# Performance work log

Measured on AMD Instinct MI355X. Metric: run time of the kernel, lower is better.

The kernel has to match this reference:

```python
import jax, jax.numpy as jnp
import numpy as np

C = 256  # channels
B, H, W = 16, 64, 64


def _conv1x1(x, w, b):
    # x: [B,Cin,H,W], w: [Cout,Cin], b: [Cout] -> [B,Cout,H,W]
    return jnp.einsum('bchw,oc->bohw', x, w) + b[None, :, None, None]


def _axis_attn(x, wq, bq, wf, bf, axis):
    # axis: -1 for 'W', -2 for 'H'
    qkv = _conv1x1(x, wq, bq)                      # [B,1+2C,H,W]
    query = qkv[:, :1]                             # [B,1,H,W]
    key = qkv[:, 1:1 + C]                          # [B,C,H,W]
    value = qkv[:, 1 + C:]                         # [B,C,H,W]
    scores = jax.nn.softmax(query, axis=axis)      # softmax over spatial axis
    context = jnp.sum(key * scores, axis=axis, keepdims=True)  # [B,C,H,1] or [B,C,1,W]
    gate = jax.nn.sigmoid(value)
    out = x + gate * context                       # broadcast over reduced axis
    return _conv1x1(out, wf, bf)


def setup_inputs() -> dict:
    key = jax.random.key(0)
    ks = jax.random.split(key, 5)
    s_qkv = 1.0 / np.sqrt(C)
    s_fus = 1.0 / np.sqrt(C)
    return {
        'x': jax.random.normal(ks[0], (B, C, H, W), dtype=jnp.float32),
        'qkvW_w': jax.random.normal(ks[1], (1 + 2 * C, C), dtype=jnp.float32) * s_qkv,
        'qkvW_b': jnp.zeros((1 + 2 * C,), dtype=jnp.float32),
        'qkvH_w': jax.random.normal(ks[2], (1 + 2 * C, C), dtype=jnp.float32) * s_qkv,
        'qkvH_b': jnp.zeros((1 + 2 * C,), dtype=jnp.float32),
        'fusW_w': jax.random.normal(ks[3], (C, C), dtype=jnp.float32) * s_fus,
        'fusW_b': jnp.zeros((C,), dtype=jnp.float32),
        'fusH_w': jax.random.normal(ks[4], (C, C), dtype=jnp.float32) * s_fus,
        'fusH_b': jnp.zeros((C,), dtype=jnp.float32),
    }


def reference(x, qkvW_w, qkvW_b, qkvH_w, qkvH_b, fusW_w, fusW_b, fusH_w, fusH_b):
    x_w = _axis_attn(x, qkvW_w, qkvW_b, fusW_w, fusW_b, axis=-1)
    x_h = _axis_attn(x_w, qkvH_w, qkvH_b, fusH_w, fusH_b, axis=-2)
    return x_h
```

## Files before the change

kernel.cpp:

```cpp
#include <hip/hip_runtime.h>

typedef unsigned short u16;
typedef unsigned int u32;
typedef __attribute__((ext_vector_type(8))) short bf16x8;
typedef __attribute__((ext_vector_type(4))) float f32x4;

__device__ __forceinline__ u16 f2bf(float f) {
    u32 u = __builtin_bit_cast(u32, f);
    u += 0x7FFFu + ((u >> 16) & 1u);
    return (u16)(u >> 16);
}
__device__ __forceinline__ float bf2f(u16 s) {
    u32 u = ((u32)s) << 16;
    return __builtin_bit_cast(float, u);
}
__device__ __forceinline__ float sigm(float x) {
    return 1.0f / (1.0f + __expf(-x));
}
__device__ __forceinline__ void gload16(const u16* g, u16* l) {
    __builtin_amdgcn_global_load_lds(
        (const __attribute__((address_space(1))) void*)g,
        (__attribute__((address_space(3))) void*)l, 16, 0, 0);
}

__global__ __launch_bounds__(256) void transpose_in(const float* __restrict__ x,
                                                    u16* __restrict__ xp) {
    __shared__ float tile[64][65];
    int bid = blockIdx.x;
    int ct = bid & 3, h = (bid >> 2) & 63, b = bid >> 8;
    int t = threadIdx.x;
    int tr = t >> 4, tc = t & 15;
    const float* src = x + (((size_t)(b * 256 + ct * 64) * 64 + h) * 64);
#pragma unroll
    for (int i = 0; i < 4; ++i) {
        int c = tr + i * 16;
        float4 v = *(const float4*)(src + (size_t)c * 4096 + tc * 4);
        tile[c][tc * 4 + 0] = v.x;
        tile[c][tc * 4 + 1] = v.y;
        tile[c][tc * 4 + 2] = v.z;
        tile[c][tc * 4 + 3] = v.w;
    }
    __syncthreads();
    u16* dst = xp + ((size_t)((b * 64 + h) * 64)) * 256 + ct * 64;
#pragma unroll
    for (int i = 0; i < 4; ++i) {
        int w = tr + i * 16;
        ushort4 o;
        o.x = f2bf(tile[tc * 4 + 0][w]);
        o.y = f2bf(tile[tc * 4 + 1][w]);
        o.z = f2bf(tile[tc * 4 + 2][w]);
        o.w = f2bf(tile[tc * 4 + 3][w]);
        *(ushort4*)(dst + (size_t)w * 256 + tc * 4) = o;
    }
}

__global__ __launch_bounds__(256) void prep_w(const float* __restrict__ qw,
                                              const float* __restrict__ qb,
                                              const float* __restrict__ fw,
                                              const float* __restrict__ fb,
                                              float* __restrict__ wq0,
                                              u16* __restrict__ wkv,
                                              float* __restrict__ bkv,
                                              u16* __restrict__ wf,
                                              float* __restrict__ bff) {
    int i = blockIdx.x * 256 + threadIdx.x;
    if (i < 513 * 256) {
        int o = i >> 8, c = i & 255;
        float v = qw[i];
        if (o == 0) wq0[c] = v;
        else        wkv[(size_t)(o - 1) * 256 + c] = f2bf(v);
    }
    if (i < 65536) wf[i] = f2bf(fw[i]);
    if (i < 512)   bkv[i] = qb[i + 1];
    if (i < 256)   bff[i] = fb[i];
}

template <int AXIS>
__global__ __launch_bounds__(512, 4) void qkv_attn(
    const u16* __restrict__ A, const u16* __restrict__ Bw,
    const float* __restrict__ bkv, const float* __restrict__ wq0,
    u16* __restrict__ G) {
    __shared__ alignas(16) u16 Asm[128 * 256];
    __shared__ float ql[128];
    __shared__ float sc[128];
    __shared__ alignas(16) float ctxs[2][256];
    int t = threadIdx.x, lane = t & 63, wv = t >> 6;
    int beta = blockIdx.x;
    auto prow = [&](int r) -> size_t {
        if (AXIS == 0) return (size_t)beta * 128 + r;
        else           return (size_t)(beta >> 5) * 4096 + (size_t)(r & 63) * 64 +
                              ((beta & 31) * 2) + (r >> 6);
    };
    {
#pragma unroll
        for (int i = 0; i < 8; ++i) {
            int row = i * 16 + wv * 2 + (lane >> 5);
            int slot = (lane & 31) ^ (row & 7);
            gload16(A + prow(row) * 256 + slot * 8, &Asm[(i * 16 + wv * 2) * 256]);
        }
    }
    __syncthreads();
    {
        int row = t >> 2, g = t & 3;
        const float* wp = wq0 + g * 64;
        float a = 0.f;
#pragma unroll
        for (int cc = 0; cc < 8; ++cc) {
            int slot = (g * 8 + cc) ^ (row & 7);
            bf16x8 v = *(const bf16x8*)&Asm[row * 256 + slot * 8];
#pragma unroll
            for (int j = 0; j < 8; ++j) a += bf2f((u16)v[j]) * wp[cc * 8 + j];
        }
        a += __shfl_xor(a, 1);
        a += __shfl_xor(a, 2);
        if (g == 0) ql[row] = a;
    }
    __syncthreads();
    if (t < 128) {
        float qv = ql[t];
        float m = qv;
#pragma unroll
        for (int off = 32; off > 0; off >>= 1) m = fmaxf(m, __shfl_xor(m, off));
        float e = __expf(qv - m);
        float s = e;
#pragma unroll
        for (int off = 32; off > 0; off >>= 1) s += __shfl_xor(s, off);
        sc[t] = e / s;
    }
    __syncthreads();
    int rowhalf = wv >> 2, chq = wv & 3;
    int arow = lane & 15, kgrp = lane >> 4;
    float sv[4];
#pragma unroll
    for (int ni = 0; ni < 4; ++ni) sv[ni] = sc[rowhalf * 64 + ni * 16 + arow];
    for (int ot = 0; ot < 4; ++ot) {
        f32x4 zero = {0.f, 0.f, 0.f, 0.f};
        f32x4 acc[2][4];
#pragma unroll
        for (int mi = 0; mi < 2; ++mi)
#pragma unroll
            for (int ni = 0; ni < 4; ++ni) acc[mi][ni] = zero;
#pragma unroll
        for (int ks = 0; ks < 8; ++ks) {
            bf16x8 aw[2], bx[4];
#pragma unroll
            for (int mi = 0; mi < 2; ++mi)
                aw[mi] = *(const bf16x8*)(Bw +
                    (size_t)(ot * 128 + chq * 32 + mi * 16 + arow) * 256 +
                    ks * 32 + kgrp * 8);
#pragma unroll
            for (int ni = 0; ni < 4; ++ni) {
                int p = rowhalf * 64 + ni * 16 + arow;
                int slot = (ks * 4 + kgrp) ^ (p & 7);
                bx[ni] = *(const bf16x8*)&Asm[p * 256 + slot * 8];
            }
#pragma unroll
            for (int mi = 0; mi < 2; ++mi)
#pragma unroll
                for (int ni = 0; ni < 4; ++ni)
                    acc[mi][ni] = __builtin_amdgcn_mfma_f32_16x16x32_bf16(
                        aw[mi], bx[ni], acc[mi][ni], 0, 0, 0);
        }
        if (ot < 2) {
#pragma unroll
            for (int mi = 0; mi < 2; ++mi) {
                int c = ot * 128 + chq * 32 + mi * 16 + kgrp * 4;
                f32x4 red;
#pragma unroll
                for (int r = 0; r < 4; ++r) {
                    float s = 0.f;
#pragma unroll
                    for (int ni = 0; ni < 4; ++ni) s += acc[mi][ni][r] * sv[ni];
                    s += __shfl_xor(s, 1);
                    s += __shfl_xor(s, 2);
                    s += __shfl_xor(s, 4);
                    s += __shfl_xor(s, 8);
                    red[r] = s;
                }
                if (arow == 0) {
                    f32x4 bv = *(const f32x4*)&bkv[c];
                    red[0] += bv[0]; red[1] += bv[1];
                    red[2] += bv[2]; red[3] += bv[3];
                    *(f32x4*)&ctxs[rowhalf][c] = red;
                }
            }
        } else {
#pragma unroll
            for (int mi = 0; mi < 2; ++mi) {
                int cv = (ot - 2) * 128 + chq * 32 + mi * 16 + kgrp * 4;
                f32x4 bv = *(const f32x4*)&bkv[256 + cv];
                f32x4 cxv = *(const f32x4*)&ctxs[rowhalf][cv];
#pragma unroll
                for (int ni = 0; ni < 4; ++ni) {
                    int p = rowhalf * 64 + ni * 16 + arow;
                    int slot = (cv >> 3) ^ (p & 7);
                    ushort4 xv = *(const ushort4*)&Asm[p * 256 + slot * 8 + (cv & 7)];
                    ushort4 o;
                    o.x = f2bf(bf2f(xv.x) + sigm(acc[mi][ni][0] + bv[0]) * cxv[0]);
                    o.y = f2bf(bf2f(xv.y) + sigm(acc[mi][ni][1] + bv[1]) * cxv[1]);
                    o.z = f2bf(bf2f(xv.z) + sigm(acc[mi][ni][2] + bv[2]) * cxv[2]);
                    o.w = f2bf(bf2f(xv.w) + sigm(acc[mi][ni][3] + bv[3]) * cxv[3]);
                    *(ushort4*)(G + prow(p) * 256 + cv) = o;
                }
            }
        }
        if (ot == 1) __syncthreads();
    }
}

template <int MODE>
__global__ __launch_bounds__(256, 2) void gemm_k(
    const u16* __restrict__ A, const u16* __restrict__ Bw,
    const float* __restrict__ bias,
    u16* __restrict__ bOut, float* __restrict__ fOut) {
    int h = blockIdx.x;
    int xcd = h & 7, slot = h >> 3;
    int otile = slot & 1, ptile = xcd * 64 + (slot >> 1);
    __shared__ alignas(16) u16 Asm[128 * 64];
    __shared__ alignas(16) u16 Bsm[128 * 64];
    int p0 = ptile * 128, o0 = otile * 128;
    int t = threadIdx.x, lane = t & 63, wv = t >> 6;
    int wm = (wv >> 1) * 64, wn = (wv & 1) * 64;
    int l7 = lane & 7;
    int srcoff = (lane >> 3) * 256 + (((lane & 7) ^ (lane >> 3)) * 8);
    int arow = lane & 15, kgrp = lane >> 4;
    f32x4 zero = {0.f, 0.f, 0.f, 0.f};
    f32x4 acc[4][4];
#pragma unroll
    for (int i = 0; i < 4; ++i)
#pragma unroll
        for (int jj = 0; jj < 4; ++jj) acc[i][jj] = zero;

    for (int k0 = 0; k0 < 256; k0 += 64) {
        __syncthreads();
#pragma unroll
        for (int it = 0; it < 4; ++it) {
            int r0 = it * 32 + wv * 8;
            gload16(A + (size_t)(p0 + r0) * 256 + k0 + srcoff, &Asm[r0 * 64]);
            gload16(Bw + (size_t)(o0 + r0) * 256 + k0 + srcoff, &Bsm[r0 * 64]);
        }
        __syncthreads();
#pragma unroll
        for (int kk = 0; kk < 64; kk += 32) {
            int soff = (((kk >> 3) + kgrp) ^ l7) << 3;
            bf16x8 af[4], bfv[4];
#pragma unroll
            for (int mi = 0; mi < 4; ++mi)
                af[mi] = *(const bf16x8*)&Asm[(wm + mi * 16 + arow) * 64 + soff];
#pragma unroll
            for (int ni = 0; ni < 4; ++ni)
                bfv[ni] = *(const bf16x8*)&Bsm[(wn + ni * 16 + arow) * 64 + soff];
#pragma unroll
            for (int mi = 0; mi < 4; ++mi)
#pragma unroll
                for (int ni = 0; ni < 4; ++ni)
                    acc[mi][ni] = __builtin_amdgcn_mfma_f32_16x16x32_bf16(
                        af[mi], bfv[ni], acc[mi][ni], 0, 0, 0);
        }
    }
#pragma unroll
    for (int mi = 0; mi < 4; ++mi) {
#pragma unroll
        for (int ni = 0; ni < 4; ++ni) {
            int col = o0 + wn + ni * 16 + arow;
            float bv = bias[col];
#pragma unroll
            for (int r = 0; r < 4; ++r) {
                int row = p0 + wm + mi * 16 + ((lane >> 4) << 2) + r;
                float v = acc[mi][ni][r] + bv;
                if (MODE == 1) {
                    bOut[(size_t)row * 256 + col] = f2bf(v);
                } else {
                    fOut[((size_t)((row >> 12) * 256 + col)) * 4096 + (row & 4095)] = v;
                }
            }
        }
    }
}

extern "C" void kernel_launch(void* const* d_in, const int* in_sizes, int n_in,
                              void* d_out, int out_size, void* d_ws, size_t ws_size,
                              hipStream_t stream) {
    const float* x   = (const float*)d_in[0];
    const float* qWw = (const float*)d_in[1];
    const float* qWb = (const float*)d_in[2];
    const float* qHw = (const float*)d_in[3];
    const float* qHb = (const float*)d_in[4];
    const float* fWw = (const float*)d_in[5];
    const float* fWb = (const float*)d_in[6];
    const float* fHw = (const float*)d_in[7];
    const float* fHb = (const float*)d_in[8];
    float* out = (float*)d_out;

    char* ws = (char*)d_ws;
    size_t off = 0;
    auto carve = [&](size_t bytes) -> void* {
        off = (off + 255) & ~(size_t)255;
        void* p = ws + off;
        off += bytes;
        return p;
    };
    const size_t P = 65536;
    u16*   xp  = (u16*)carve(P * 256 * 2);
    u16*   kb  = (u16*)carve(P * 256 * 2);
    u16*   vb  = (u16*)carve(P * 256 * 2);
    float* wq01 = (float*)carve(256 * 4);
    u16*   wkv1 = (u16*)carve(512 * 256 * 2);
    float* bkv1 = (float*)carve(512 * 4);
    u16*   wf1  = (u16*)carve(65536 * 2);
    float* bf1  = (float*)carve(256 * 4);
    float* wq02 = (float*)carve(256 * 4);
    u16*   wkv2 = (u16*)carve(512 * 256 * 2);
    float* bkv2 = (float*)carve(512 * 4);
    u16*   wf2  = (u16*)carve(65536 * 2);
    float* bf2  = (float*)carve(256 * 4);

    prep_w<<<513, 256, 0, stream>>>(qWw, qWb, fWw, fWb, wq01, wkv1, bkv1, wf1, bf1);
    prep_w<<<513, 256, 0, stream>>>(qHw, qHb, fHw, fHb, wq02, wkv2, bkv2, wf2, bf2);
    transpose_in<<<4096, 256, 0, stream>>>(x, xp);

    qkv_attn<0><<<512, 512, 0, stream>>>(xp, wkv1, bkv1, wq01, kb);
    gemm_k<1><<<1024, 256, 0, stream>>>(kb, wf1, bf1, vb, nullptr);
    qkv_attn<1><<<512, 512, 0, stream>>>(vb, wkv2, bkv2, wq02, kb);
    gemm_k<2><<<1024, 256, 0, stream>>>(kb, wf2, bf2, nullptr, out);
    (void)in_sizes; (void)n_in; (void)out_size; (void)ws_size;
}
```

Before: 159.1 us.

## Compute attention context by reassociating scores before key projection

```diff
diff --git a/kernel.cpp b/kernel.cpp
--- a/kernel.cpp
+++ b/kernel.cpp
@@ -76,13 +76,14 @@
 }
 
 template <int AXIS>
-__global__ __launch_bounds__(512, 4) void qkv_attn(
+__global__ __launch_bounds__(512, 3) void qkv_attn(
     const u16* __restrict__ A, const u16* __restrict__ Bw,
     const float* __restrict__ bkv, const float* __restrict__ wq0,
     u16* __restrict__ G) {
     __shared__ alignas(16) u16 Asm[128 * 256];
     __shared__ float ql[128];
     __shared__ float sc[128];
+    __shared__ alignas(16) float ys[2][256];
     __shared__ alignas(16) float ctxs[2][256];
     int t = threadIdx.x, lane = t & 63, wv = t >> 6;
     int beta = blockIdx.x;
@@ -128,26 +129,75 @@
         sc[t] = e / s;
     }
     __syncthreads();
+    {
+        int line = t >> 8;
+        int chunk = (t & 255) >> 3;
+        int sub = t & 7;
+        float part[8] = {0.f, 0.f, 0.f, 0.f, 0.f, 0.f, 0.f, 0.f};
+#pragma unroll
+        for (int i = 0; i < 8; ++i) {
+            int row = line * 64 + sub * 8 + i;
+            int slot = chunk ^ i;
+            bf16x8 xv = *(const bf16x8*)&Asm[row * 256 + slot * 8];
+            float scp = sc[row];
+#pragma unroll
+            for (int j = 0; j < 8; ++j) part[j] += bf2f((u16)xv[j]) * scp;
+        }
+#pragma unroll
+        for (int off = 1; off < 8; off <<= 1)
+#pragma unroll
+            for (int j = 0; j < 8; ++j) part[j] += __shfl_xor(part[j], off);
+        if (sub == 0) {
+            f32x4 lo = {part[0], part[1], part[2], part[3]};
+            f32x4 hi = {part[4], part[5], part[6], part[7]};
+            *(f32x4*)&ys[line][chunk * 8] = lo;
+            *(f32x4*)&ys[line][chunk * 8 + 4] = hi;
+        }
+    }
+    __syncthreads();
+    {
+        int line = t >> 8, c = t & 255;
+        const u16* wk = Bw + (size_t)c * 256;
+        float a = 0.f;
+#pragma unroll
+        for (int kc = 0; kc < 32; ++kc) {
+            bf16x8 w = *(const bf16x8*)(wk + kc * 8);
+#pragma unroll
+            for (int j = 0; j < 8; ++j) a += bf2f((u16)w[j]) * ys[line][kc * 8 + j];
+        }
+        ctxs[line][c] = a + bkv[c];
+    }
+    __syncthreads();
     int rowhalf = wv >> 2, chq = wv & 3;
     int arow = lane & 15, kgrp = lane >> 4;
-    float sv[4];
-#pragma unroll
-    for (int ni = 0; ni < 4; ++ni) sv[ni] = sc[rowhalf * 64 + ni * 16 + arow];
-    for (int ot = 0; ot < 4; ++ot) {
-        f32x4 zero = {0.f, 0.f, 0.f, 0.f};
-        f32x4 acc[2][4];
-#pragma unroll
-        for (int mi = 0; mi < 2; ++mi)
-#pragma unroll
-            for (int ni = 0; ni < 4; ++ni) acc[mi][ni] = zero;
-#pragma unroll
-        for (int ks = 0; ks < 8; ++ks) {
-            bf16x8 aw[2], bx[4];
+    const u16* Wv = Bw + ((size_t)(256 + chq * 32 + arow)) * 256 + kgrp * 8;
+    bf16x8 wbuf[2][8];
+    auto loadgrp = [&](bf16x8(&dst)[8], int ot, int g) {
+#pragma unroll
+        for (int kk = 0; kk < 4; ++kk)
 #pragma unroll
             for (int mi = 0; mi < 2; ++mi)
-                aw[mi] = *(const bf16x8*)(Bw +
-                    (size_t)(ot * 128 + chq * 32 + mi * 16 + arow) * 256 +
-                    ks * 32 + kgrp * 8);
+                dst[kk * 2 + mi] = *(const bf16x8*)(Wv +
+                    (size_t)(ot * 128 + mi * 16) * 256 + (g * 4 + kk) * 32);
+    };
+    f32x4 zero = {0.f, 0.f, 0.f, 0.f};
+    f32x4 acc[2][4];
+    loadgrp(wbuf[0], 0, 0);
+#pragma unroll
+    for (int Gi = 0; Gi < 4; ++Gi) {
+        const int ot = Gi >> 1, g = Gi & 1;
+        if (Gi < 3) loadgrp(wbuf[(Gi + 1) & 1], (Gi + 1) >> 1, (Gi + 1) & 1);
+        __builtin_amdgcn_sched_barrier(0);
+        if (g == 0) {
+#pragma unroll
+            for (int mi = 0; mi < 2; ++mi)
+#pragma unroll
+                for (int ni = 0; ni < 4; ++ni) acc[mi][ni] = zero;
+        }
+#pragma unroll
+        for (int kk = 0; kk < 4; ++kk) {
+            int ks = g * 4 + kk;
+            bf16x8 bx[4];
 #pragma unroll
             for (int ni = 0; ni < 4; ++ni) {
                 int p = rowhalf * 64 + ni * 16 + arow;
@@ -159,35 +209,12 @@
 #pragma unroll
                 for (int ni = 0; ni < 4; ++ni)
                     acc[mi][ni] = __builtin_amdgcn_mfma_f32_16x16x32_bf16(
-                        aw[mi], bx[ni], acc[mi][ni], 0, 0, 0);
-        }
-        if (ot < 2) {
+                        wbuf[Gi & 1][kk * 2 + mi], bx[ni], acc[mi][ni], 0, 0, 0);
+        }
+        if (g == 1) {
 #pragma unroll
             for (int mi = 0; mi < 2; ++mi) {
-                int c = ot * 128 + chq * 32 + mi * 16 + kgrp * 4;
-                f32x4 red;
-#pragma unroll
-                for (int r = 0; r < 4; ++r) {
-                    float s = 0.f;
-#pragma unroll
-                    for (int ni = 0; ni < 4; ++ni) s += acc[mi][ni][r] * sv[ni];
-                    s += __shfl_xor(s, 1);
-                    s += __shfl_xor(s, 2);
-                    s += __shfl_xor(s, 4);
-                    s += __shfl_xor(s, 8);
-                    red[r] = s;
-                }
-                if (arow == 0) {
-                    f32x4 bv = *(const f32x4*)&bkv[c];
-                    red[0] += bv[0]; red[1] += bv[1];
-                    red[2] += bv[2]; red[3] += bv[3];
-                    *(f32x4*)&ctxs[rowhalf][c] = red;
-                }
-            }
-        } else {
-#pragma unroll
-            for (int mi = 0; mi < 2; ++mi) {
-                int cv = (ot - 2) * 128 + chq * 32 + mi * 16 + kgrp * 4;
+                int cv = ot * 128 + chq * 32 + mi * 16 + kgrp * 4;
                 f32x4 bv = *(const f32x4*)&bkv[256 + cv];
                 f32x4 cxv = *(const f32x4*)&ctxs[rowhalf][cv];
 #pragma unroll
@@ -204,7 +231,6 @@
                 }
             }
         }
-        if (ot == 1) __syncthreads();
     }
 }
 
```

New measurement: 183.2 us. 15.1% more time.

## Compute attention context by reducing input before key projection

Applied to the files above, without the earlier changes.

```diff
diff --git a/kernel.cpp b/kernel.cpp
--- a/kernel.cpp
+++ b/kernel.cpp
@@ -83,6 +83,7 @@
     __shared__ alignas(16) u16 Asm[128 * 256];
     __shared__ float ql[128];
     __shared__ float sc[128];
+    __shared__ alignas(16) float ys[2][256];
     __shared__ alignas(16) float ctxs[2][256];
     int t = threadIdx.x, lane = t & 63, wv = t >> 6;
     int beta = blockIdx.x;
@@ -128,12 +129,35 @@
         sc[t] = e / s;
     }
     __syncthreads();
+    {
+        int line = t >> 8, c = t & 255;
+        int chunk = c >> 3, e7 = c & 7;
+        int rbase = line * 64;
+        float a = 0.f;
+#pragma unroll 8
+        for (int p = 0; p < 64; ++p) {
+            int slot = chunk ^ (p & 7);
+            a += bf2f(Asm[(rbase + p) * 256 + slot * 8 + e7]) * sc[rbase + p];
+        }
+        ys[line][c] = a;
+    }
+    __syncthreads();
+    {
+        int line = t >> 8, c = t & 255;
+        const u16* wk = Bw + (size_t)c * 256;
+        float a = 0.f;
+#pragma unroll
+        for (int kc = 0; kc < 32; ++kc) {
+            bf16x8 w = *(const bf16x8*)(wk + kc * 8);
+#pragma unroll
+            for (int j = 0; j < 8; ++j) a += bf2f((u16)w[j]) * ys[line][kc * 8 + j];
+        }
+        ctxs[line][c] = a + bkv[c];
+    }
+    __syncthreads();
     int rowhalf = wv >> 2, chq = wv & 3;
     int arow = lane & 15, kgrp = lane >> 4;
-    float sv[4];
-#pragma unroll
-    for (int ni = 0; ni < 4; ++ni) sv[ni] = sc[rowhalf * 64 + ni * 16 + arow];
-    for (int ot = 0; ot < 4; ++ot) {
+    for (int ot = 2; ot < 4; ++ot) {
         f32x4 zero = {0.f, 0.f, 0.f, 0.f};
         f32x4 acc[2][4];
 #pragma unroll
@@ -161,50 +185,24 @@
                     acc[mi][ni] = __builtin_amdgcn_mfma_f32_16x16x32_bf16(
                         aw[mi], bx[ni], acc[mi][ni], 0, 0, 0);
         }
-        if (ot < 2) {
-#pragma unroll
-            for (int mi = 0; mi < 2; ++mi) {
-                int c = ot * 128 + chq * 32 + mi * 16 + kgrp * 4;
-                f32x4 red;
-#pragma unroll
-                for (int r = 0; r < 4; ++r) {
-                    float s = 0.f;
-#pragma unroll
-                    for (int ni = 0; ni < 4; ++ni) s += acc[mi][ni][r] * sv[ni];
-                    s += __shfl_xor(s, 1);
-                    s += __shfl_xor(s, 2);
-                    s += __shfl_xor(s, 4);
-                    s += __shfl_xor(s, 8);
-                    red[r] = s;
-                }
-                if (arow == 0) {
-                    f32x4 bv = *(const f32x4*)&bkv[c];
-                    red[0] += bv[0]; red[1] += bv[1];
-                    red[2] += bv[2]; red[3] += bv[3];
-                    *(f32x4*)&ctxs[rowhalf][c] = red;
-                }
+#pragma unroll
+        for (int mi = 0; mi < 2; ++mi) {
+            int cv = (ot - 2) * 128 + chq * 32 + mi * 16 + kgrp * 4;
+            f32x4 bv = *(const f32x4*)&bkv[256 + cv];
+            f32x4 cxv = *(const f32x4*)&ctxs[rowhalf][cv];
+#pragma unroll
+            for (int ni = 0; ni < 4; ++ni) {
+                int p = rowhalf * 64 + ni * 16 + arow;
+                int slot = (cv >> 3) ^ (p & 7);
+                ushort4 xv = *(const ushort4*)&Asm[p * 256 + slot * 8 + (cv & 7)];
+                ushort4 o;
+                o.x = f2bf(bf2f(xv.x) + sigm(acc[mi][ni][0] + bv[0]) * cxv[0]);
+                o.y = f2bf(bf2f(xv.y) + sigm(acc[mi][ni][1] + bv[1]) * cxv[1]);
+                o.z = f2bf(bf2f(xv.z) + sigm(acc[mi][ni][2] + bv[2]) * cxv[2]);
+                o.w = f2bf(bf2f(xv.w) + sigm(acc[mi][ni][3] + bv[3]) * cxv[3]);
+                *(ushort4*)(G + prow(p) * 256 + cv) = o;
             }
-        } else {
-#pragma unroll
-            for (int mi = 0; mi < 2; ++mi) {
-                int cv = (ot - 2) * 128 + chq * 32 + mi * 16 + kgrp * 4;
-                f32x4 bv = *(const f32x4*)&bkv[256 + cv];
-                f32x4 cxv = *(const f32x4*)&ctxs[rowhalf][cv];
-#pragma unroll
-                for (int ni = 0; ni < 4; ++ni) {
-                    int p = rowhalf * 64 + ni * 16 + arow;
-                    int slot = (cv >> 3) ^ (p & 7);
-                    ushort4 xv = *(const ushort4*)&Asm[p * 256 + slot * 8 + (cv & 7)];
-                    ushort4 o;
-                    o.x = f2bf(bf2f(xv.x) + sigm(acc[mi][ni][0] + bv[0]) * cxv[0]);
-                    o.y = f2bf(bf2f(xv.y) + sigm(acc[mi][ni][1] + bv[1]) * cxv[1]);
-                    o.z = f2bf(bf2f(xv.z) + sigm(acc[mi][ni][2] + bv[2]) * cxv[2]);
-                    o.w = f2bf(bf2f(xv.w) + sigm(acc[mi][ni][3] + bv[3]) * cxv[3]);
-                    *(ushort4*)(G + prow(p) * 256 + cv) = o;
-                }
-            }
-        }
-        if (ot == 1) __syncthreads();
+        }
     }
 }
 
```

Result: slower. 242.9 us (+52.6%).
